# Performance work log

Hardware: AMD Instinct MI355X
Metric: run time of the kernel (lower is better)

## Reference

```python
import jax, jax.numpy as jnp
import numpy as np
from jax import lax

B, T, D = 8, 2048, 1024
DECAY = 0.99
EPS = 1e-5


def _layer_norm(x, w, b):
    mu = jnp.mean(x, axis=-1, keepdims=True)
    var = jnp.var(x, axis=-1, keepdims=True)
    return (x - mu) * lax.rsqrt(var + EPS) * w + b


def _fixed_decay_scan(v, decay):
    # h_t = decay * h_{t-1} + v_t along axis=1, h_0 = v_0 (zero initial state)
    a = jnp.full_like(v, decay)

    def combine(c1, c2):
        a1, b1 = c1
        a2, b2 = c2
        return (a1 * a2, a2 * b1 + b2)

    _, h = lax.associative_scan(combine, (a, v), axis=1)
    return h


def setup_inputs() -> dict:
    key = jax.random.key(0)
    ks = jax.random.split(key, 12)
    s = 0.02
    return {
        "x": jax.random.normal(ks[0], (B, T, D), dtype=jnp.float32),
        "mask": jnp.ones((B, T), dtype=jnp.float32),
        "ln1_w": jnp.ones((D,), jnp.float32),
        "ln1_b": jnp.zeros((D,), jnp.float32),
        "ln2_w": jnp.ones((D,), jnp.float32),
        "ln2_b": jnp.zeros((D,), jnp.float32),
        "Wg_f": jax.random.normal(ks[1], (D, D), jnp.float32) * s,
        "bg_f": jnp.ones((D,), jnp.float32),
        "Wg_b": jax.random.normal(ks[2], (D, D), jnp.float32) * s,
        "bg_b": jnp.ones((D,), jnp.float32),
        "W_fuse": jax.random.normal(ks[3], (2 * D, D), jnp.float32) * s,
        "b_fuse": jnp.zeros((D,), jnp.float32),
        "W_ffn1": jax.random.normal(ks[4], (D, 2 * D), jnp.float32) * s,
        "b_ffn1": jnp.zeros((2 * D,), jnp.float32),
        "W_ffn2": jax.random.normal(ks[5], (2 * D, D), jnp.float32) * s,
        "b_ffn2": jnp.zeros((D,), jnp.float32),
    }


def reference(x, mask, ln1_w, ln1_b, ln2_w, ln2_b, Wg_f, bg_f, Wg_b, bg_b,
              W_fuse, b_fuse, W_ffn1, b_ffn1, W_ffn2, b_ffn2):
    residual = x
    h = _layer_norm(x, ln1_w, ln1_b)
    m = mask[..., None]  # (B,T,1)

    # forward-direction gated scan
    v_fwd = jax.nn.sigmoid(h @ Wg_f + bg_f) * h * m
    h_fwd = _fixed_decay_scan(v_fwd, DECAY)

    # backward-direction gated scan (scan over reversed time)
    v_bwd = jax.nn.sigmoid(h @ Wg_b + bg_b) * h * m
    h_bwd = jnp.flip(_fixed_decay_scan(jnp.flip(v_bwd, axis=1), DECAY), axis=1)

    # learned fusion gate
    beta = jax.nn.sigmoid(jnp.concatenate([h_fwd, h_bwd], axis=-1) @ W_fuse + b_fuse)
    fused = beta * h_fwd + (1.0 - beta) * h_bwd

    x = residual + fused  # dropout is identity in eval mode

    # FFN block (exact GELU as torch nn.GELU default)
    ffn = jax.nn.gelu(_layer_norm(x, ln2_w, ln2_b) @ W_ffn1 + b_ffn1, approximate=False) @ W_ffn2 + b_ffn2
    return x + ffn
```

## Files before the change

### kernel.cpp

```cpp
#include <hip/hip_runtime.h>
#include <math.h>

#define Bq 8
#define Tq 2048
#define Dq 1024
#define Mq (Bq*Tq)
#define NCHq 32
#define CHUNKq 64
#define DECAYq 0.99f
#define DF64q 0.52559646f
#define SGq (Bq*NCHq*4)
#define CEBNDq ((size_t)Bq*NCHq*Dq)

typedef unsigned short u16;
typedef unsigned int u32;
typedef __attribute__((ext_vector_type(8))) short bf16x8;
typedef __attribute__((ext_vector_type(4))) float f32x4;
typedef __attribute__((ext_vector_type(4))) u16 u16x4;

__device__ __forceinline__ u16 f2bf(float f) {
  u32 u = __builtin_bit_cast(u32, f);
  return (u16)((u + 0x7FFFu + ((u >> 16) & 1u)) >> 16);
}
__device__ __forceinline__ float bf2f(u16 h) {
  return __builtin_bit_cast(float, (u32)h << 16);
}
__device__ __forceinline__ float sigm(float x) { return 1.0f / (1.0f + expf(-x)); }

__global__ __launch_bounds__(256)
void transpose_all(const float* __restrict__ s0, u16* __restrict__ d0,
                   const float* __restrict__ s1, u16* __restrict__ d1,
                   const float* __restrict__ s2, u16* __restrict__ d2,
                   const float* __restrict__ s3, u16* __restrict__ d3,
                   const float* __restrict__ s4, u16* __restrict__ d4) {
  const int bid = blockIdx.x;
  const float* src; u16* dst; int K, N, local;
  if (bid < 1024)      { src = s0; dst = d0; K = 1024; N = 1024; local = bid; }
  else if (bid < 2048) { src = s1; dst = d1; K = 1024; N = 1024; local = bid - 1024; }
  else if (bid < 4096) { src = s2; dst = d2; K = 2048; N = 1024; local = bid - 2048; }
  else if (bid < 6144) { src = s3; dst = d3; K = 1024; N = 2048; local = bid - 4096; }
  else                 { src = s4; dst = d4; K = 2048; N = 1024; local = bid - 6144; }
  const int ntx = N >> 5;
  const int n0 = (local % ntx) << 5;
  const int k0 = (local / ntx) << 5;
  __shared__ float tile[32][33];
  const int tx = threadIdx.x & 31;
  const int ty = threadIdx.x >> 5;
#pragma unroll
  for (int j = 0; j < 32; j += 8)
    tile[ty + j][tx] = src[(size_t)(k0 + ty + j) * N + (n0 + tx)];
  __syncthreads();
#pragma unroll
  for (int j = 0; j < 32; j += 8)
    dst[(size_t)(n0 + ty + j) * K + (k0 + tx)] = f2bf(tile[tx][ty + j]);
}

__global__ __launch_bounds__(256)
void ln_kernel(const float* __restrict__ xin, const float* __restrict__ w,
               const float* __restrict__ bb, u16* __restrict__ obf) {
  const int row = blockIdx.x;
  const int tid = threadIdx.x;
  const float4 v = ((const float4*)(xin + (size_t)row * Dq))[tid];
  float s  = v.x + v.y + v.z + v.w;
  float s2 = v.x*v.x + v.y*v.y + v.z*v.z + v.w*v.w;
#pragma unroll
  for (int o = 32; o > 0; o >>= 1) { s += __shfl_xor(s, o); s2 += __shfl_xor(s2, o); }
  __shared__ float rs[4], rq[4];
  const int wid = tid >> 6;
  if ((tid & 63) == 0) { rs[wid] = s; rq[wid] = s2; }
  __syncthreads();
  s  = rs[0] + rs[1] + rs[2] + rs[3];
  s2 = rq[0] + rq[1] + rq[2] + rq[3];
  const float mu  = s * (1.0f/Dq);
  const float var = s2 * (1.0f/Dq) - mu*mu;
  const float inv = rsqrtf(var + 1e-5f);
  const float4 wv = ((const float4*)w)[tid];
  const float4 bv = ((const float4*)bb)[tid];
  float4 o;
  o.x = (v.x - mu)*inv*wv.x + bv.x;
  o.y = (v.y - mu)*inv*wv.y + bv.y;
  o.z = (v.z - mu)*inv*wv.z + bv.z;
  o.w = (v.w - mu)*inv*wv.w + bv.w;
  u16x4 ob; ob[0] = f2bf(o.x); ob[1] = f2bf(o.y); ob[2] = f2bf(o.z); ob[3] = f2bf(o.w);
  ((u16x4*)(obf + (size_t)row * Dq))[tid] = ob;
}

__global__ __launch_bounds__(256)
void ln_bf_kernel(const u16* __restrict__ xin, const float* __restrict__ w,
                  const float* __restrict__ bb, u16* __restrict__ obf) {
  const int row = blockIdx.x;
  const int tid = threadIdx.x;
  const u16x4 vu = ((const u16x4*)(xin + (size_t)row * Dq))[tid];
  float v0 = bf2f(vu[0]), v1 = bf2f(vu[1]), v2 = bf2f(vu[2]), v3 = bf2f(vu[3]);
  float s  = v0 + v1 + v2 + v3;
  float s2 = v0*v0 + v1*v1 + v2*v2 + v3*v3;
#pragma unroll
  for (int o = 32; o > 0; o >>= 1) { s += __shfl_xor(s, o); s2 += __shfl_xor(s2, o); }
  __shared__ float rs[4], rq[4];
  const int wid = tid >> 6;
  if ((tid & 63) == 0) { rs[wid] = s; rq[wid] = s2; }
  __syncthreads();
  s  = rs[0] + rs[1] + rs[2] + rs[3];
  s2 = rq[0] + rq[1] + rq[2] + rq[3];
  const float mu  = s * (1.0f/Dq);
  const float var = s2 * (1.0f/Dq) - mu*mu;
  const float inv = rsqrtf(var + 1e-5f);
  const float4 wv = ((const float4*)w)[tid];
  const float4 bv = ((const float4*)bb)[tid];
  u16x4 ob;
  ob[0] = f2bf((v0 - mu)*inv*wv.x + bv.x);
  ob[1] = f2bf((v1 - mu)*inv*wv.y + bv.y);
  ob[2] = f2bf((v2 - mu)*inv*wv.z + bv.z);
  ob[3] = f2bf((v3 - mu)*inv*wv.w + bv.w);
  ((u16x4*)(obf + (size_t)row * Dq))[tid] = ob;
}

__global__ __launch_bounds__(256)
void scan_pass1_dual(const u16* __restrict__ vf, const u16* __restrict__ vb,
                     float* __restrict__ ce) {
  int bid = blockIdx.x;
  const bool rev = bid >= SGq;
  if (rev) bid -= SGq;
  const int dblk = bid & 3;
  const int c    = (bid >> 2) & 31;
  const int b    = bid >> 7;
  const int d    = (dblk << 8) + threadIdx.x;
  const u16* v   = rev ? vb : vf;
  float* cep     = ce + (rev ? CEBNDq : 0);
  const long step = rev ? -(long)Dq : (long)Dq;
  size_t idx = ((size_t)b * Tq + (rev ? (Tq - 1 - c * CHUNKq) : c * CHUNKq)) * Dq + d;
  float e = 0.0f;
  for (int i = 0; i < CHUNKq; ++i) { e = DECAYq * e + bf2f(v[idx]); idx += step; }
  cep[((size_t)b * NCHq + c) * Dq + d] = e;
}

__global__ __launch_bounds__(256)
void scan_pass2_dual(const float* __restrict__ ce, float* __restrict__ car) {
  const int idx = blockIdx.x * 256 + threadIdx.x;
  const int dir = idx >> 13;
  const int loc = idx & 8191;
  const int b = loc >> 10;
  const int d = loc & 1023;
  const size_t base = (size_t)dir * CEBNDq;
  float c = 0.0f;
  for (int k = 0; k < NCHq; ++k) {
    const size_t i = base + ((size_t)b * NCHq + k) * Dq + d;
    car[i] = c;
    c = DF64q * c + ce[i];
  }
}

__global__ __launch_bounds__(256)
void scan_pass3_dual(u16* __restrict__ vf, u16* __restrict__ vb,
                     const float* __restrict__ car) {
  int bid = blockIdx.x;
  const bool rev = bid >= SGq;
  if (rev) bid -= SGq;
  const int dblk = bid & 3;
  const int c    = (bid >> 2) & 31;
  const int b    = bid >> 7;
  const int d    = (dblk << 8) + threadIdx.x;
  u16* v = rev ? vb : vf;
  const float* carp = car + (rev ? CEBNDq : 0);
  float hc = carp[((size_t)b * NCHq + c) * Dq + d];
  const long step = rev ? -(long)Dq : (long)Dq;
  size_t idx = ((size_t)b * Tq + (rev ? (Tq - 1 - c * CHUNKq) : c * CHUNKq)) * Dq + d;
  for (int i = 0; i < CHUNKq; ++i) {
    hc = DECAYq * hc + bf2f(v[idx]);
    v[idx] = f2bf(hc);
    idx += step;
  }
}

struct EpiGate {
  const u16* h; const float* mask; const float* bgf; const float* bgb;
  u16* vf; u16* vb;
  __device__ void operator()(int r, int c, float val) const {
    const bool fwd = c < 1024;
    const int cc = c & 1023;
    const float s = sigm(val + (fwd ? bgf[cc] : bgb[cc]));
    const float hv = bf2f(h[(size_t)r * Dq + cc]) * mask[r];
    (fwd ? vf : vb)[(size_t)r * Dq + cc] = f2bf(s * hv);
  }
};
struct EpiFuse {
  const float* bfuse; const float* x; const u16* hf; const u16* hb; u16* x2;
  __device__ void operator()(int r, int c, float val) const {
    const size_t i = (size_t)r * Dq + c;
    const float bta = sigm(val + bfuse[c]);
    x2[i] = f2bf(x[i] + bta * bf2f(hf[i]) + (1.0f - bta) * bf2f(hb[i]));
  }
};
struct EpiFfn1 {
  const float* b1; u16* a;
  __device__ void operator()(int r, int c, float val) const {
    const float u = val + b1[c];
    const float g = 0.5f * u * (1.0f + erff(u * 0.70710678118f));
    a[(size_t)r * 2048 + c] = f2bf(g);
  }
};
struct EpiFfn2 {
  const float* b2; const u16* x2; float* o;
  __device__ void operator()(int r, int c, float val) const {
    const size_t i = (size_t)r * Dq + c;
    o[i] = val + b2[c] + bf2f(x2[i]);
  }
};

template<typename Epi>
__global__ __launch_bounds__(512)
void gemm_bt(const u16* __restrict__ A, const u16* __restrict__ A2, int ksplit,
             const u16* __restrict__ BT, int K, int nx, Epi epi) {
  __shared__ u16 As[2][8192];
  __shared__ u16 Bs[2][8192];
  const int tid  = threadIdx.x;
  const int lane = tid & 63;
  const int w    = tid >> 6;
  const int wr   = w >> 2;
  const int wc   = w & 3;

  const int lin = blockIdx.x;
  const int q8  = gridDim.x >> 3;
  const int t   = (lin & 7) * q8 + (lin >> 3);
  const int by  = t / nx;
  const int bx  = t - by * nx;
  const int rowBase = by << 7;
  const int colBase = bx << 7;

  const int srow  = tid >> 3;
  const int scolE = (((tid & 7) ^ (srow & 7)) << 4) >> 1;
  const int KA    = (ksplit < K) ? ksplit : K;

  auto stage = [&](int buf, int kt) {
    const int kbase = kt << 6;
    const u16* Abase = (kbase < ksplit) ? A : A2;
    const int  kA    = (kbase < ksplit) ? kbase : (kbase - ksplit);
#pragma unroll
    for (int qq = 0; qq < 2; ++qq) {
      const u16* ga = Abase + (size_t)(rowBase + (qq << 6) + srow) * KA + kA + scolE;
      const u16* gb = BT    + (size_t)(colBase + (qq << 6) + srow) * K + kbase + scolE;
      __builtin_amdgcn_global_load_lds(
          (const __attribute__((address_space(1))) void*)ga,
          (__attribute__((address_space(3))) void*)(&As[buf][0] + (qq << 12) + (w << 9)), 16, 0, 0);
      __builtin_amdgcn_global_load_lds(
          (const __attribute__((address_space(1))) void*)gb,
          (__attribute__((address_space(3))) void*)(&Bs[buf][0] + (qq << 12) + (w << 9)), 16, 0, 0);
    }
  };

  f32x4 acc[4][2];
#pragma unroll
  for (int m = 0; m < 4; ++m)
#pragma unroll
    for (int n = 0; n < 2; ++n) acc[m][n] = (f32x4){0.f, 0.f, 0.f, 0.f};

  const int nkt = K >> 6;
  stage(0, 0);
  asm volatile("s_waitcnt vmcnt(0)" ::: "memory");
  __builtin_amdgcn_s_barrier();

  int cur = 0;
  for (int kt = 0; kt < nkt; ++kt) {
    if (kt + 1 < nkt) stage(cur ^ 1, kt + 1);
    const char* Ab = (const char*)&As[cur][0];
    const char* Bb = (const char*)&Bs[cur][0];
#pragma unroll
    for (int kk = 0; kk < 2; ++kk) {
      bf16x8 af[4], bfr[2];
      const int cb = (kk << 6) + ((lane >> 4) << 4);
#pragma unroll
      for (int m = 0; m < 4; ++m) {
        const int r = (wr << 6) + (m << 4) + (lane & 15);
        af[m] = *(const bf16x8*)(Ab + (r << 7) + (cb ^ ((r & 7) << 4)));
      }
#pragma unroll
      for (int n = 0; n < 2; ++n) {
        const int r = (wc << 5) + (n << 4) + (lane & 15);
        bfr[n] = *(const bf16x8*)(Bb + (r << 7) + (cb ^ ((r & 7) << 4)));
      }
#pragma unroll
      for (int m = 0; m < 4; ++m)
#pragma unroll
        for (int n = 0; n < 2; ++n)
          acc[m][n] = __builtin_amdgcn_mfma_f32_16x16x32_bf16(af[m], bfr[n], acc[m][n], 0, 0, 0);
    }
    __builtin_amdgcn_sched_barrier(0);
    asm volatile("s_waitcnt vmcnt(0) lgkmcnt(0)" ::: "memory");
    __builtin_amdgcn_s_barrier();
    cur ^= 1;
  }

#pragma unroll
  for (int m = 0; m < 4; ++m) {
    const int grow0 = rowBase + (wr << 6) + (m << 4) + ((lane >> 4) << 2);
#pragma unroll
    for (int n = 0; n < 2; ++n) {
      const int gcol = colBase + (wc << 5) + (n << 4) + (lane & 15);
#pragma unroll
      for (int r2 = 0; r2 < 4; ++r2)
        epi(grow0 + r2, gcol, acc[m][n][r2]);
    }
  }
}

extern "C" void kernel_launch(void* const* d_in, const int* in_sizes, int n_in,
                              void* d_out, int out_size, void* d_ws, size_t ws_size,
                              hipStream_t stream) {
  (void)in_sizes; (void)n_in; (void)out_size; (void)ws_size;
  const float* x      = (const float*)d_in[0];
  const float* mask   = (const float*)d_in[1];
  const float* ln1w   = (const float*)d_in[2];
  const float* ln1b   = (const float*)d_in[3];
  const float* ln2w   = (const float*)d_in[4];
  const float* ln2b   = (const float*)d_in[5];
  const float* Wg_f   = (const float*)d_in[6];
  const float* bg_f   = (const float*)d_in[7];
  const float* Wg_b   = (const float*)d_in[8];
  const float* bg_b   = (const float*)d_in[9];
  const float* W_fuse = (const float*)d_in[10];
  const float* b_fuse = (const float*)d_in[11];
  const float* W_ffn1 = (const float*)d_in[12];
  const float* b_ffn1 = (const float*)d_in[13];
  const float* W_ffn2 = (const float*)d_in[14];
  const float* b_ffn2 = (const float*)d_in[15];
  float* out = (float*)d_out;

  char* ws = (char*)d_ws;
  size_t off = 0;
  auto alloc = [&](size_t bytes) { char* p = ws + off; off += (bytes + 255) & ~(size_t)255; return p; };
  u16*   x2     = (u16*)  alloc((size_t)Mq * Dq * 2);
  u16*   slotA  = (u16*)  alloc((size_t)Mq * Dq * 2);
  u16*   hf_bf  = (u16*)  alloc((size_t)Mq * Dq * 2);
  u16*   hb_bf  = (u16*)  alloc((size_t)Mq * Dq * 2);
  u16*   WgT    = (u16*)  alloc((size_t)2048 * 1024 * 2);
  u16*   WfuT   = (u16*)  alloc((size_t)1024 * 2048 * 2);
  u16*   Wf1T   = (u16*)  alloc((size_t)2048 * 1024 * 2);
  u16*   Wf2T   = (u16*)  alloc((size_t)1024 * 2048 * 2);
  float* ce     = (float*)alloc(2 * CEBNDq * 4);
  float* car    = (float*)alloc(2 * CEBNDq * 4);
  u16*   h_bf16 = slotA;
  u16*   y2     = slotA;
  u16*   a_bf16 = hf_bf;

  transpose_all<<<8192, 256, 0, stream>>>(Wg_f, WgT, Wg_b, WgT + 1024 * 1024,
                                          W_fuse, WfuT, W_ffn1, Wf1T, W_ffn2, Wf2T);

  ln_kernel<<<Mq, 256, 0, stream>>>(x, ln1w, ln1b, h_bf16);

  EpiGate eg{h_bf16, mask, bg_f, bg_b, hf_bf, hb_bf};
  gemm_bt<EpiGate><<<16 * (Mq / 128), 512, 0, stream>>>(h_bf16, h_bf16, 1024, WgT, 1024, 16, eg);

  scan_pass1_dual<<<2 * SGq, 256, 0, stream>>>(hf_bf, hb_bf, ce);
  scan_pass2_dual<<<64, 256, 0, stream>>>(ce, car);
  scan_pass3_dual<<<2 * SGq, 256, 0, stream>>>(hf_bf, hb_bf, car);

  EpiFuse ef{b_fuse, x, hf_bf, hb_bf, x2};
  gemm_bt<EpiFuse><<<8 * (Mq / 128), 512, 0, stream>>>(hf_bf, hb_bf, 1024, WfuT, 2048, 8, ef);

  ln_bf_kernel<<<Mq, 256, 0, stream>>>(x2, ln2w, ln2b, y2);

  EpiFfn1 e1{b_ffn1, a_bf16};
  gemm_bt<EpiFfn1><<<16 * (Mq / 128), 512, 0, stream>>>(y2, y2, 1024, Wf1T, 1024, 16, e1);

  EpiFfn2 e2{b_ffn2, x2, out};
  gemm_bt<EpiFfn2><<<8 * (Mq / 128), 512, 0, stream>>>(a_bf16, a_bf16, 2048, Wf2T, 2048, 8, e2);
}
```

Measured before the change: 499.4 us.

## Halve GEMM K-tile to 32 with packed two-row LDS layout for occupancy

Shrinks the GEMM's per-stage K tile from 64 to 32, halving shared memory per block. Two logical rows are packed into each 128-byte LDS row, with a matching swizzle and a single async load per thread. It also adds a min-blocks hint to launch_bounds so more blocks can be resident. The aim is to hide latency through occupancy, at the cost of twice as many barriers and loop iterations per K and less MFMA work between syncs.

```diff
diff --git a/kernel.cpp b/kernel.cpp
--- a/kernel.cpp
+++ b/kernel.cpp
@@ -208,11 +208,11 @@
 };
 
 template<typename Epi>
-__global__ __launch_bounds__(512)
+__global__ __launch_bounds__(512, 8)
 void gemm_bt(const u16* __restrict__ A, const u16* __restrict__ A2, int ksplit,
              const u16* __restrict__ BT, int K, int nx, Epi epi) {
-  __shared__ u16 As[2][8192];
-  __shared__ u16 Bs[2][8192];
+  __shared__ u16 As[2][4096];
+  __shared__ u16 Bs[2][4096];
   const int tid  = threadIdx.x;
   const int lane = tid & 63;
   const int w    = tid >> 6;
@@ -227,25 +227,24 @@
   const int rowBase = by << 7;
   const int colBase = bx << 7;
 
-  const int srow  = tid >> 3;
-  const int scolE = (((tid & 7) ^ (srow & 7)) << 4) >> 1;
-  const int KA    = (ksplit < K) ? ksplit : K;
+  const int p_  = tid >> 3;
+  const int sp  = (tid & 7) ^ (p_ & 7);
+  const int lr  = (p_ << 1) + (sp >> 2);
+  const int ce_ = (sp & 3) << 3;
+  const int KA  = (ksplit < K) ? ksplit : K;
 
   auto stage = [&](int buf, int kt) {
-    const int kbase = kt << 6;
+    const int kbase = kt << 5;
     const u16* Abase = (kbase < ksplit) ? A : A2;
     const int  kA    = (kbase < ksplit) ? kbase : (kbase - ksplit);
-#pragma unroll
-    for (int qq = 0; qq < 2; ++qq) {
-      const u16* ga = Abase + (size_t)(rowBase + (qq << 6) + srow) * KA + kA + scolE;
-      const u16* gb = BT    + (size_t)(colBase + (qq << 6) + srow) * K + kbase + scolE;
-      __builtin_amdgcn_global_load_lds(
-          (const __attribute__((address_space(1))) void*)ga,
-          (__attribute__((address_space(3))) void*)(&As[buf][0] + (qq << 12) + (w << 9)), 16, 0, 0);
-      __builtin_amdgcn_global_load_lds(
-          (const __attribute__((address_space(1))) void*)gb,
-          (__attribute__((address_space(3))) void*)(&Bs[buf][0] + (qq << 12) + (w << 9)), 16, 0, 0);
-    }
+    const u16* ga = Abase + (size_t)(rowBase + lr) * KA + kA + ce_;
+    const u16* gb = BT    + (size_t)(colBase + lr) * K + kbase + ce_;
+    __builtin_amdgcn_global_load_lds(
+        (const __attribute__((address_space(1))) void*)ga,
+        (__attribute__((address_space(3))) void*)((char*)&As[buf][0] + (tid << 4)), 16, 0, 0);
+    __builtin_amdgcn_global_load_lds(
+        (const __attribute__((address_space(1))) void*)gb,
+        (__attribute__((address_space(3))) void*)((char*)&Bs[buf][0] + (tid << 4)), 16, 0, 0);
   };
 
   f32x4 acc[4][2];
@@ -254,36 +253,37 @@
 #pragma unroll
     for (int n = 0; n < 2; ++n) acc[m][n] = (f32x4){0.f, 0.f, 0.f, 0.f};
 
-  const int nkt = K >> 6;
+  const int nkt = K >> 5;
   stage(0, 0);
   asm volatile("s_waitcnt vmcnt(0)" ::: "memory");
   __builtin_amdgcn_s_barrier();
 
+  const int g16 = (lane >> 4) << 4;
   int cur = 0;
   for (int kt = 0; kt < nkt; ++kt) {
     if (kt + 1 < nkt) stage(cur ^ 1, kt + 1);
     const char* Ab = (const char*)&As[cur][0];
     const char* Bb = (const char*)&Bs[cur][0];
-#pragma unroll
-    for (int kk = 0; kk < 2; ++kk) {
-      bf16x8 af[4], bfr[2];
-      const int cb = (kk << 6) + ((lane >> 4) << 4);
-#pragma unroll
-      for (int m = 0; m < 4; ++m) {
-        const int r = (wr << 6) + (m << 4) + (lane & 15);
-        af[m] = *(const bf16x8*)(Ab + (r << 7) + (cb ^ ((r & 7) << 4)));
-      }
-#pragma unroll
-      for (int n = 0; n < 2; ++n) {
-        const int r = (wc << 5) + (n << 4) + (lane & 15);
-        bfr[n] = *(const bf16x8*)(Bb + (r << 7) + (cb ^ ((r & 7) << 4)));
-      }
-#pragma unroll
-      for (int m = 0; m < 4; ++m)
-#pragma unroll
-        for (int n = 0; n < 2; ++n)
-          acc[m][n] = __builtin_amdgcn_mfma_f32_16x16x32_bf16(af[m], bfr[n], acc[m][n], 0, 0, 0);
+    bf16x8 af[4], bfr[2];
+#pragma unroll
+    for (int m = 0; m < 4; ++m) {
+      const int r  = (wr << 6) + (m << 4) + (lane & 15);
+      const int pr = r >> 1;
+      const int c  = (((r & 1) << 6) + g16) ^ ((pr & 7) << 4);
+      af[m] = *(const bf16x8*)(Ab + (pr << 7) + c);
     }
+#pragma unroll
+    for (int n = 0; n < 2; ++n) {
+      const int r  = (wc << 5) + (n << 4) + (lane & 15);
+      const int pr = r >> 1;
+      const int c  = (((r & 1) << 6) + g16) ^ ((pr & 7) << 4);
+      bfr[n] = *(const bf16x8*)(Bb + (pr << 7) + c);
+    }
+#pragma unroll
+    for (int m = 0; m < 4; ++m)
+#pragma unroll
+      for (int n = 0; n < 2; ++n)
+        acc[m][n] = __builtin_amdgcn_mfma_f32_16x16x32_bf16(af[m], bfr[n], acc[m][n], 0, 0, 0);
     __builtin_amdgcn_sched_barrier(0);
     asm volatile("s_waitcnt vmcnt(0) lgkmcnt(0)" ::: "memory");
     __builtin_amdgcn_s_barrier();
```

New measurement: 532.4 us. 6.6% more time.
